# Kernel tuning notes

Measured on AMD Instinct MI355X. Metric: run time of the kernel, lower is better.

The kernel has to match this reference:

```python
import jax, jax.numpy as jnp
import numpy as np

GRID = 256

def _build_edges(g):
    ii, jj = np.meshgrid(np.arange(g), np.arange(g), indexing='ij')
    center = ii * g + jj
    srcs, tgts, attrs = [], [], []
    for di in (-1, 0, 1):
        for dj in (-1, 0, 1):
            if di == 0 and dj == 0:
                continue
            ni, nj = ii + di, jj + dj
            m = (ni >= 0) & (ni < g) & (nj >= 0) & (nj < g)
            srcs.append(center[m])
            tgts.append((ni * g + nj)[m])
            n = int(m.sum())
            a = np.empty((n, 3), np.float32)
            a[:, 0] = np.sqrt(di * di + dj * dj)
            a[:, 1] = di
            a[:, 2] = dj
            attrs.append(a)
    return (np.concatenate(srcs).astype(np.int32),
            np.concatenate(tgts).astype(np.int32),
            np.concatenate(attrs, axis=0))

def setup_inputs() -> dict:
    key = jax.random.key(0)
    ks = jax.random.split(key, 16)
    B, T, C, g = 2, 5, 10, GRID
    width, kw, out_c, Hh = 64, 32, 10, 32
    src, tgt, attr = _build_edges(g)
    nrm = lambda k, s: 0.1 * jax.random.normal(k, s, dtype=jnp.float32)
    return {
        'x': nrm(ks[0], (B, T, C, g, g)),
        'edge_src': jnp.asarray(src),
        'edge_tgt': jnp.asarray(tgt),
        'edge_attr': jnp.asarray(attr),
        'Wih0': nrm(ks[1], (4 * Hh, C)),
        'Whh0': nrm(ks[2], (4 * Hh, Hh)),
        'bih0': nrm(ks[3], (4 * Hh,)),
        'bhh0': nrm(ks[4], (4 * Hh,)),
        'Wih1': nrm(ks[5], (4 * Hh, Hh)),
        'Whh1': nrm(ks[6], (4 * Hh, Hh)),
        'bih1': nrm(ks[7], (4 * Hh,)),
        'bhh1': nrm(ks[8], (4 * Hh,)),
        'fc1_w': nrm(ks[9], (width, Hh)),
        'fc1_b': nrm(ks[10], (width,)),
        'conv_w': nrm(ks[11], (4, width, width)),
        'conv_b': nrm(ks[12], (4, width)),
        'gparam': jnp.ones((4,), jnp.float32),
        'fc2_w': nrm(ks[13], (kw, width)),
        'fc2_b': nrm(ks[14], (kw,)),
        'fc3_w': nrm(ks[15], (out_c, kw)),
        'fc3_b': jnp.zeros((out_c,), jnp.float32),
    }

def _lstm_cell(xt, h, c, Wih, Whh, bih, bhh):
    z = xt @ Wih.T + bih + h @ Whh.T + bhh
    i, f, g, o = jnp.split(z, 4, axis=-1)  # torch gate order i,f,g,o
    c = jax.nn.sigmoid(f) * c + jax.nn.sigmoid(i) * jnp.tanh(g)
    h = jax.nn.sigmoid(o) * jnp.tanh(c)
    return h, c

def _forward(x, edge_src, edge_tgt, edge_attr, Wih0, Whh0, bih0, bhh0,
             Wih1, Whh1, bih1, bhh1, fc1_w, fc1_b, conv_w, conv_b, gparam,
             fc2_w, fc2_b, fc3_w, fc3_b):
    B, T, C, H, W = x.shape
    N = H * W
    Hh = Whh0.shape[1]
    # (B,T,C,H,W) -> (T, B*N, C) sequence for the temporal LSTM over every node
    seq = x.transpose(0, 3, 4, 1, 2).reshape(B * N, T, C).transpose(1, 0, 2)

    def step(carry, xt):
        h0, c0, h1, c1 = carry
        h0, c0 = _lstm_cell(xt, h0, c0, Wih0, Whh0, bih0, bhh0)
        h1, c1 = _lstm_cell(h0, h1, c1, Wih1, Whh1, bih1, bhh1)
        return (h0, c0, h1, c1), None

    z = jnp.zeros((B * N, Hh), x.dtype)
    (h0, c0, h1, c1), _ = jax.lax.scan(step, (z, z, z, z), seq)
    feats = jax.nn.relu(h1 @ fc1_w.T + fc1_b).reshape(B, N, -1)  # (B,N,width)

    dist2 = edge_attr[:, 0:1] ** 2  # (E,1)
    depth = conv_w.shape[0]
    for k in range(depth):
        gw = jnp.exp(-dist2 / (gparam[k] ** 2 + 1e-8))       # (E,1) gaussian gate
        msg = (feats[:, edge_src] @ conv_w[k]) * gw          # (B,E,width)
        agg = jnp.zeros_like(feats).at[:, edge_tgt].add(msg) # scatter-add per batch
        feats = agg + feats @ conv_w[k] + conv_b[k]
        if k != depth - 1:
            feats = jax.nn.relu(feats)

    out = jax.nn.relu(feats @ fc2_w.T + fc2_b) @ fc3_w.T + fc3_b  # (B,N,out_c)
    out = out.reshape(B, H, W, -1).transpose(0, 3, 1, 2)[:, None]  # (B,1,out_c,H,W)
    return out

def reference(x, edge_src, edge_tgt, edge_attr, Wih0, Whh0, bih0, bhh0,
              Wih1, Whh1, bih1, bhh1, fc1_w, fc1_b, conv_w, conv_b, gparam,
              fc2_w, fc2_b, fc3_w, fc3_b):
    return _forward(x, edge_src, edge_tgt, edge_attr, Wih0, Whh0, bih0, bhh0,
                    Wih1, Whh1, bih1, bhh1, fc1_w, fc1_b, conv_w, conv_b, gparam,
                    fc2_w, fc2_b, fc3_w, fc3_b)
```

## Files before the change

### kernel.cpp

```cpp
#include <hip/hip_runtime.h>
#include <hip/hip_bf16.h>

#define NPIX   65536
#define TT     5
#define CC     10
#define HH     32
#define WIDTH  64
#define KW     32
#define OUTC   10

#define OFF_L0I    0
#define OFF_L0H    1280
#define OFF_L1I    5376
#define OFF_L1H    9472
#define OFF_B0     13568
#define OFF_B1     13696
#define OFF_FC1W   13824
#define OFF_FC1B   15872
#define OFF_CWT2   16384
#define OFF_CB     32768
#define OFF_FC2W2  33024
#define OFF_FC2B   35072
#define OFF_FC3W4  35104
#define OFF_FC3B   35424
#define OFF_GW     35440
#define OFF_FEATS_A 36864
#define OFF_FEATS_B (36864 + 8388608)

#define STRAIGHT_ATTR_IDX (65025 * 3)

__device__ __forceinline__ float sigf(float x)  { return 1.0f / (1.0f + __expf(-x)); }
__device__ __forceinline__ float tanhf_(float x){ return 1.0f - 2.0f / (__expf(2.0f * x) + 1.0f); }

__global__ __launch_bounds__(256, 1)
void prep_kernel(const float* Wih0, const float* Whh0,
                 const float* bih0, const float* bhh0,
                 const float* Wih1, const float* Whh1,
                 const float* bih1, const float* bhh1,
                 const float* fc1w, const float* fc1b,
                 const float* convw, const float* convb,
                 const float* fc2w, const float* fc2b,
                 const float* fc3w, const float* fc3b,
                 const float* gparam, const float* eattr,
                 float* P) {
    int tid = blockIdx.x * blockDim.x + threadIdx.x;
    int stride = gridDim.x * blockDim.x;
    for (int idx = tid; idx < 1280; idx += stride) {
        int g = idx & 3, j = (idx >> 2) & 31, c = idx >> 7;
        P[OFF_L0I + idx] = Wih0[(g * 32 + j) * 10 + c];
    }
    for (int idx = tid; idx < 4096; idx += stride) {
        int g = idx & 3, j = (idx >> 2) & 31, k = idx >> 7;
        P[OFF_L0H + idx] = Whh0[(g * 32 + j) * 32 + k];
        P[OFF_L1I + idx] = Wih1[(g * 32 + j) * 32 + k];
        P[OFF_L1H + idx] = Whh1[(g * 32 + j) * 32 + k];
    }
    for (int idx = tid; idx < 128; idx += stride) {
        int g = idx & 3, j = idx >> 2;
        P[OFF_B0 + idx] = bih0[g * 32 + j] + bhh0[g * 32 + j];
        P[OFF_B1 + idx] = bih1[g * 32 + j] + bhh1[g * 32 + j];
    }
    for (int idx = tid; idx < 2048; idx += stride) {
        int ch = idx & 63, k = idx >> 6;
        P[OFF_FC1W + idx] = fc1w[ch * 32 + k];
    }
    for (int i = tid; i < 64; i += stride) P[OFF_FC1B + i] = fc1b[i];
    for (int idx = tid; idx < 16384; idx += stride) {
        int k = idx >> 12, r = idx & 4095, e = r >> 1, h = r & 1;
        int co2 = e >> 6, ci = e & 63;
        P[OFF_CWT2 + idx] = convw[k * 4096 + ci * 64 + (2 * co2 + h)];
    }
    for (int i = tid; i < 256; i += stride) P[OFF_CB + i] = convb[i];
    for (int idx = tid; idx < 2048; idx += stride) {
        int e = idx >> 1, h = idx & 1, m2 = e >> 6, ch = e & 63;
        P[OFF_FC2W2 + idx] = fc2w[(2 * m2 + h) * 64 + ch];
    }
    for (int i = tid; i < 32;  i += stride) P[OFF_FC2B + i] = fc2b[i];
    for (int idx = tid; idx < 320; idx += stride) {
        int q = idx & 3, e = idx >> 2, oc2 = e >> 4, m2 = e & 15;
        int oc = 2 * oc2 + (q & 1), m = 2 * m2 + (q >> 1);
        P[OFF_FC3W4 + idx] = fc3w[oc * 32 + m];
    }
    for (int i = tid; i < 10; i += stride) P[OFF_FC3B + i] = fc3b[i];
    for (int idx = tid; idx < 8; idx += stride) {
        int k = idx >> 1;
        float g = gparam[k];
        float denom = g * g + 1e-8f;
        float a = (idx & 1) ? eattr[0] : eattr[STRAIGHT_ATTR_IDX];
        P[OFF_GW + idx] = __expf(-(a * a) / denom);
    }
}

#define ROW_ACC(WBASE, SVAL) do {                                   \
    const float* wr_ = (WBASE); float sv_ = (SVAL);                 \
    _Pragma("unroll")                                               \
    for (int j_ = 0; j_ < 16; j_++) {                               \
        z[j_].x = __builtin_fmaf(wr_[4 * j_ + 0], sv_, z[j_].x);    \
        z[j_].y = __builtin_fmaf(wr_[4 * j_ + 1], sv_, z[j_].y);    \
        z[j_].z = __builtin_fmaf(wr_[4 * j_ + 2], sv_, z[j_].z);    \
        z[j_].w = __builtin_fmaf(wr_[4 * j_ + 3], sv_, z[j_].w);    \
    } } while (0)

__global__ __launch_bounds__(256, 1)
void lstm_fc1_kernel(const float* __restrict__ x,
                     const float* __restrict__ P,
                     float* __restrict__ feats) {
    __shared__ float H0[HH * 128];
    __shared__ float H1[HH * 128];

    int tid  = threadIdx.x;
    int half = __builtin_amdgcn_readfirstlane(tid >> 7);
    int pxl  = tid & 127;
    int hw   = half << 4;
    int hw4  = half << 6;

    int n = blockIdx.x * 128 + pxl;
    int b = n >> 16;
    int pix = n & (NPIX - 1);
    const float* xb = x + (size_t)b * TT * CC * NPIX + pix;

    float c0[16], c1[16];
#pragma unroll
    for (int j = 0; j < 16; j++) {
        c0[j] = 0.f; c1[j] = 0.f;
        H0[(hw + j) * 128 + pxl] = 0.f;
        H1[(hw + j) * 128 + pxl] = 0.f;
    }
    __syncthreads();

#pragma unroll 1
    for (int t = 0; t < TT; t++) {
        float xcur[CC];
#pragma unroll
        for (int c = 0; c < CC; c++)
            xcur[c] = xb[(size_t)(t * CC + c) * NPIX];

        {
            float4 z[16];
            const float* bb = P + OFF_B0 + hw4;
#pragma unroll
            for (int j = 0; j < 16; j++)
                z[j] = *(const float4*)(bb + 4 * j);
#pragma unroll 1
            for (int c = 0; c < CC; c++)
                ROW_ACC(P + OFF_L0I + c * 128 + hw4, xcur[c]);
#pragma unroll 1
            for (int k = 0; k < HH; k++) {
                float hv = H0[k * 128 + pxl];
                ROW_ACC(P + OFF_L0H + k * 128 + hw4, hv);
            }
            __syncthreads();
#pragma unroll
            for (int j = 0; j < 16; j++) {
                float cn = sigf(z[j].y) * c0[j] + sigf(z[j].x) * tanhf_(z[j].z);
                c0[j] = cn;
                H0[(hw + j) * 128 + pxl] = sigf(z[j].w) * tanhf_(cn);
            }
            __syncthreads();
        }

        {
            float4 z[16];
            const float* bb = P + OFF_B1 + hw4;
#pragma unroll
            for (int j = 0; j < 16; j++)
                z[j] = *(const float4*)(bb + 4 * j);
#pragma unroll 1
            for (int k = 0; k < HH; k++) {
                float hv = H0[k * 128 + pxl];
                ROW_ACC(P + OFF_L1I + k * 128 + hw4, hv);
            }
#pragma unroll 1
            for (int k = 0; k < HH; k++) {
                float hv = H1[k * 128 + pxl];
                ROW_ACC(P + OFF_L1H + k * 128 + hw4, hv);
            }
            __syncthreads();
#pragma unroll
            for (int j = 0; j < 16; j++) {
                float cn = sigf(z[j].y) * c1[j] + sigf(z[j].x) * tanhf_(z[j].z);
                c1[j] = cn;
                H1[(hw + j) * 128 + pxl] = sigf(z[j].w) * tanhf_(cn);
            }
            __syncthreads();
        }
    }

    float f[32];
    {
        const float* fb1 = P + OFF_FC1B + (half << 5);
#pragma unroll
        for (int m = 0; m < 32; m++) f[m] = fb1[m];
    }
#pragma unroll 1
    for (int k = 0; k < HH; k++) {
        float hv = H1[k * 128 + pxl];
        const float* wr = P + OFF_FC1W + k * 64 + (half << 5);
#pragma unroll
        for (int m = 0; m < 32; m++)
            f[m] = __builtin_fmaf(wr[m], hv, f[m]);
    }
    float* fob = feats + (size_t)b * WIDTH * NPIX + (size_t)(half * 32) * NPIX + pix;
#pragma unroll
    for (int m = 0; m < 32; m++)
        fob[(size_t)m * NPIX] = fmaxf(f[m], 0.f);
}

__global__ __launch_bounds__(256, 1)
void conv_fused_kernel(const float* __restrict__ Fin, float* __restrict__ Fout,
                       const float* __restrict__ P, int k) {
    __shared__ float4 CW[1024];
    __shared__ float  CB[64];
    {
        const float4* src = (const float4*)(P + OFF_CWT2 + k * 4096);
        for (int i = threadIdx.x; i < 1024; i += 256) CW[i] = src[i];
        if (threadIdx.x < 64) CB[threadIdx.x] = P[OFF_CB + k * 64 + threadIdx.x];
    }
    __syncthreads();

    int n = blockIdx.x * 256 + threadIdx.x;
    int b = n >> 16;
    int pix = n & (NPIX - 1);
    int i = pix >> 8, j = pix & 255;
    float wstr = P[OFF_GW + 2 * k], wdiag = P[OFF_GW + 2 * k + 1];
    float fu = (i > 0) ? wstr : 0.f, fd = (i < 255) ? wstr : 0.f;
    float fl = (j > 0) ? wstr : 0.f, fr = (j < 255) ? wstr : 0.f;
    float ful = (i > 0 && j > 0) ? wdiag : 0.f, fur = (i > 0 && j < 255) ? wdiag : 0.f;
    float fdl = (i < 255 && j > 0) ? wdiag : 0.f, fdr = (i < 255 && j < 255) ? wdiag : 0.f;

    const float* fb = Fin + (size_t)b * WIDTH * NPIX + pix;
    float u[WIDTH];
#pragma unroll
    for (int ch = 0; ch < WIDTH; ch++) {
        const float* yc = fb + (size_t)ch * NPIX;
        float v = yc[0];
        v += fu * yc[-256] + fd * yc[256] + fl * yc[-1] + fr * yc[1];
        v += ful * yc[-257] + fur * yc[-255] + fdl * yc[255] + fdr * yc[257];
        u[ch] = v;
    }

    float* ob = Fout + (size_t)b * WIDTH * NPIX + pix;
#pragma unroll 1
    for (int co2 = 0; co2 < 32; co2++) {
        float ax = CB[2 * co2], ay = CB[2 * co2 + 1];
        const float4* wv = CW + co2 * 32;
#pragma unroll
        for (int ci2 = 0; ci2 < 32; ci2++) {
            float4 q = wv[ci2];
            float a0 = u[2 * ci2], a1 = u[2 * ci2 + 1];
            ax = __builtin_fmaf(q.x, a0, ax); ax = __builtin_fmaf(q.z, a1, ax);
            ay = __builtin_fmaf(q.y, a0, ay); ay = __builtin_fmaf(q.w, a1, ay);
        }
        ob[(size_t)(2 * co2) * NPIX]     = fmaxf(ax, 0.f);
        ob[(size_t)(2 * co2 + 1) * NPIX] = fmaxf(ay, 0.f);
    }
}

__global__ __launch_bounds__(256, 1)
void conv_head_kernel(const float* __restrict__ Fin, const float* __restrict__ P,
                      float* __restrict__ out) {
    const int k = 3;
    __shared__ float4 CW3[1024];
    __shared__ float  CB3[64];
    __shared__ float4 F2W[512];
    __shared__ float  F2B[32];
    __shared__ float4 F3W[80];
    __shared__ float  F3B[12];
    {
        const float4* s1 = (const float4*)(P + OFF_CWT2 + k * 4096);
        for (int i = threadIdx.x; i < 1024; i += 256) CW3[i] = s1[i];
        const float4* s2 = (const float4*)(P + OFF_FC2W2);
        for (int i = threadIdx.x; i < 512; i += 256) F2W[i] = s2[i];
        const float4* s3 = (const float4*)(P + OFF_FC3W4);
        if (threadIdx.x < 80) F3W[threadIdx.x] = s3[threadIdx.x];
        if (threadIdx.x < 64) CB3[threadIdx.x] = P[OFF_CB + k * 64 + threadIdx.x];
        if (threadIdx.x < 32) F2B[threadIdx.x] = P[OFF_FC2B + threadIdx.x];
        if (threadIdx.x < 10) F3B[threadIdx.x] = P[OFF_FC3B + threadIdx.x];
    }
    __syncthreads();

    int n = blockIdx.x * 256 + threadIdx.x;
    int b = n >> 16;
    int pix = n & (NPIX - 1);
    int i = pix >> 8, j = pix & 255;
    float wstr = P[OFF_GW + 2 * k], wdiag = P[OFF_GW + 2 * k + 1];
    float fu = (i > 0) ? wstr : 0.f, fd = (i < 255) ? wstr : 0.f;
    float fl = (j > 0) ? wstr : 0.f, fr = (j < 255) ? wstr : 0.f;
    float ful = (i > 0 && j > 0) ? wdiag : 0.f, fur = (i > 0 && j < 255) ? wdiag : 0.f;
    float fdl = (i < 255 && j > 0) ? wdiag : 0.f, fdr = (i < 255 && j < 255) ? wdiag : 0.f;

    const float* fb = Fin + (size_t)b * WIDTH * NPIX + pix;
    float u[WIDTH];
#pragma unroll
    for (int ch = 0; ch < WIDTH; ch++) {
        const float* yc = fb + (size_t)ch * NPIX;
        float v = yc[0];
        v += fu * yc[-256] + fd * yc[256] + fl * yc[-1] + fr * yc[1];
        v += ful * yc[-257] + fur * yc[-255] + fdl * yc[255] + fdr * yc[257];
        u[ch] = v;
    }

    float f[WIDTH];
#pragma unroll
    for (int co2 = 0; co2 < 32; co2++) {
        float ax = CB3[2 * co2], ay = CB3[2 * co2 + 1];
        const float4* wv = CW3 + co2 * 32;
#pragma unroll
        for (int ci2 = 0; ci2 < 32; ci2++) {
            float4 q = wv[ci2];
            float a0 = u[2 * ci2], a1 = u[2 * ci2 + 1];
            ax = __builtin_fmaf(q.x, a0, ax); ax = __builtin_fmaf(q.z, a1, ax);
            ay = __builtin_fmaf(q.y, a0, ay); ay = __builtin_fmaf(q.w, a1, ay);
        }
        f[2 * co2] = ax; f[2 * co2 + 1] = ay;
    }

    float2 oo[5];
#pragma unroll
    for (int oc2 = 0; oc2 < 5; oc2++) oo[oc2] = make_float2(F3B[2 * oc2], F3B[2 * oc2 + 1]);
#pragma unroll 1
    for (int m2 = 0; m2 < 16; m2++) {
        float ax = F2B[2 * m2], ay = F2B[2 * m2 + 1];
        const float4* wv = F2W + m2 * 32;
#pragma unroll
        for (int ch2 = 0; ch2 < 32; ch2++) {
            float4 q = wv[ch2];
            ax = __builtin_fmaf(q.x, f[2 * ch2], ax); ax = __builtin_fmaf(q.z, f[2 * ch2 + 1], ax);
            ay = __builtin_fmaf(q.y, f[2 * ch2], ay); ay = __builtin_fmaf(q.w, f[2 * ch2 + 1], ay);
        }
        ax = fmaxf(ax, 0.f); ay = fmaxf(ay, 0.f);
#pragma unroll
        for (int oc2 = 0; oc2 < 5; oc2++) {
            float4 q = F3W[oc2 * 16 + m2];
            oo[oc2].x += q.x * ax + q.z * ay;
            oo[oc2].y += q.y * ax + q.w * ay;
        }
    }
    float* ob = out + (size_t)b * OUTC * NPIX + pix;
#pragma unroll
    for (int oc2 = 0; oc2 < 5; oc2++) {
        ob[(size_t)(2 * oc2) * NPIX]     = oo[oc2].x;
        ob[(size_t)(2 * oc2 + 1) * NPIX] = oo[oc2].y;
    }
}

extern "C" void kernel_launch(void* const* d_in, const int* in_sizes, int n_in,
                              void* d_out, int out_size, void* d_ws, size_t ws_size,
                              hipStream_t stream) {
    const float* x     = (const float*)d_in[0];
    const float* eattr = (const float*)d_in[3];
    const float* Wih0  = (const float*)d_in[4];
    const float* Whh0  = (const float*)d_in[5];
    const float* bih0  = (const float*)d_in[6];
    const float* bhh0  = (const float*)d_in[7];
    const float* Wih1  = (const float*)d_in[8];
    const float* Whh1  = (const float*)d_in[9];
    const float* bih1  = (const float*)d_in[10];
    const float* bhh1  = (const float*)d_in[11];
    const float* fc1w  = (const float*)d_in[12];
    const float* fc1b  = (const float*)d_in[13];
    const float* convw = (const float*)d_in[14];
    const float* convb = (const float*)d_in[15];
    const float* gparam= (const float*)d_in[16];
    const float* fc2w  = (const float*)d_in[17];
    const float* fc2b  = (const float*)d_in[18];
    const float* fc3w  = (const float*)d_in[19];
    const float* fc3b  = (const float*)d_in[20];

    float* P  = (float*)d_ws;
    float* FA = P + OFF_FEATS_A;
    float* FB = P + OFF_FEATS_B;

    prep_kernel<<<64, 256, 0, stream>>>(Wih0, Whh0, bih0, bhh0, Wih1, Whh1, bih1, bhh1,
                                        fc1w, fc1b, convw, convb, fc2w, fc2b, fc3w, fc3b,
                                        gparam, eattr, P);
    lstm_fc1_kernel<<<1024, 256, 0, stream>>>(x, P, FA);
    conv_fused_kernel<<<512, 256, 0, stream>>>(FA, FB, P, 0);
    conv_fused_kernel<<<512, 256, 0, stream>>>(FB, FA, P, 1);
    conv_fused_kernel<<<512, 256, 0, stream>>>(FA, FB, P, 2);
    conv_head_kernel<<<512, 256, 0, stream>>>(FB, P, (float*)d_out);
}
```

Before: 654.5 us.

## Use packed float2 FMAs in LSTM and shrink blocks to 128 threads

The LSTM/fc1 kernel's gate and fc1 accumulations now use 2-wide vector FMA (v2f elementwise fma), which can map to packed FP32 FMA instructions on CDNA. The block size also drops from 256 to 128 threads (64 pixels per block, 2048 blocks), with the shared hidden-state buffers shrunk to match. The aim is to halve the FMA instruction count and allow finer-grained scheduling. The risk is that packed ops need operands in even register pairs, which could add moves, and smaller blocks mean more redundant weight loads.

Result: faster. 600.4 us (-8.3%).

```diff
diff --git a/kernel.cpp b/kernel.cpp
--- a/kernel.cpp
+++ b/kernel.cpp
@@ -29,6 +29,8 @@
 
 #define STRAIGHT_ATTR_IDX (65025 * 3)
 
+typedef float v2f __attribute__((ext_vector_type(2)));
+
 __device__ __forceinline__ float sigf(float x)  { return 1.0f / (1.0f + __expf(-x)); }
 __device__ __forceinline__ float tanhf_(float x){ return 1.0f - 2.0f / (__expf(2.0f * x) + 1.0f); }
 
@@ -91,30 +93,29 @@
     }
 }
 
-#define ROW_ACC(WBASE, SVAL) do {                                   \
-    const float* wr_ = (WBASE); float sv_ = (SVAL);                 \
-    _Pragma("unroll")                                               \
-    for (int j_ = 0; j_ < 16; j_++) {                               \
-        z[j_].x = __builtin_fmaf(wr_[4 * j_ + 0], sv_, z[j_].x);    \
-        z[j_].y = __builtin_fmaf(wr_[4 * j_ + 1], sv_, z[j_].y);    \
-        z[j_].z = __builtin_fmaf(wr_[4 * j_ + 2], sv_, z[j_].z);    \
-        z[j_].w = __builtin_fmaf(wr_[4 * j_ + 3], sv_, z[j_].w);    \
+#define ROW_ACC(WBASE, SVAL) do {                                        \
+    const v2f* wr_ = (const v2f*)(WBASE);                                \
+    float s_ = (SVAL); v2f sv_ = {s_, s_};                               \
+    _Pragma("unroll")                                                    \
+    for (int j_ = 0; j_ < 16; j_++) {                                    \
+        zA[j_] = __builtin_elementwise_fma(wr_[2 * j_],     sv_, zA[j_]);\
+        zB[j_] = __builtin_elementwise_fma(wr_[2 * j_ + 1], sv_, zB[j_]);\
     } } while (0)
 
-__global__ __launch_bounds__(256, 1)
+__global__ __launch_bounds__(128, 1)
 void lstm_fc1_kernel(const float* __restrict__ x,
                      const float* __restrict__ P,
                      float* __restrict__ feats) {
-    __shared__ float H0[HH * 128];
-    __shared__ float H1[HH * 128];
+    __shared__ float H0[HH * 64];
+    __shared__ float H1[HH * 64];
 
     int tid  = threadIdx.x;
-    int half = __builtin_amdgcn_readfirstlane(tid >> 7);
-    int pxl  = tid & 127;
+    int half = __builtin_amdgcn_readfirstlane(tid >> 6);
+    int pxl  = tid & 63;
     int hw   = half << 4;
     int hw4  = half << 6;
 
-    int n = blockIdx.x * 128 + pxl;
+    int n = blockIdx.x * 64 + pxl;
     int b = n >> 16;
     int pix = n & (NPIX - 1);
     const float* xb = x + (size_t)b * TT * CC * NPIX + pix;
@@ -123,8 +124,8 @@
 #pragma unroll
     for (int j = 0; j < 16; j++) {
         c0[j] = 0.f; c1[j] = 0.f;
-        H0[(hw + j) * 128 + pxl] = 0.f;
-        H1[(hw + j) * 128 + pxl] = 0.f;
+        H0[(hw + j) * 64 + pxl] = 0.f;
+        H1[(hw + j) * 64 + pxl] = 0.f;
     }
     __syncthreads();
 
@@ -136,74 +137,81 @@
             xcur[c] = xb[(size_t)(t * CC + c) * NPIX];
 
         {
-            float4 z[16];
-            const float* bb = P + OFF_B0 + hw4;
-#pragma unroll
-            for (int j = 0; j < 16; j++)
-                z[j] = *(const float4*)(bb + 4 * j);
+            v2f zA[16], zB[16];
+            const v2f* bb = (const v2f*)(P + OFF_B0 + hw4);
+#pragma unroll
+            for (int j = 0; j < 16; j++) {
+                zA[j] = bb[2 * j];
+                zB[j] = bb[2 * j + 1];
+            }
 #pragma unroll 1
             for (int c = 0; c < CC; c++)
                 ROW_ACC(P + OFF_L0I + c * 128 + hw4, xcur[c]);
 #pragma unroll 1
             for (int k = 0; k < HH; k++) {
-                float hv = H0[k * 128 + pxl];
+                float hv = H0[k * 64 + pxl];
                 ROW_ACC(P + OFF_L0H + k * 128 + hw4, hv);
             }
             __syncthreads();
 #pragma unroll
             for (int j = 0; j < 16; j++) {
-                float cn = sigf(z[j].y) * c0[j] + sigf(z[j].x) * tanhf_(z[j].z);
+                float cn = sigf(zA[j].y) * c0[j] + sigf(zA[j].x) * tanhf_(zB[j].x);
                 c0[j] = cn;
-                H0[(hw + j) * 128 + pxl] = sigf(z[j].w) * tanhf_(cn);
+                H0[(hw + j) * 64 + pxl] = sigf(zB[j].y) * tanhf_(cn);
             }
             __syncthreads();
         }
 
         {
-            float4 z[16];
-            const float* bb = P + OFF_B1 + hw4;
-#pragma unroll
-            for (int j = 0; j < 16; j++)
-                z[j] = *(const float4*)(bb + 4 * j);
+            v2f zA[16], zB[16];
+            const v2f* bb = (const v2f*)(P + OFF_B1 + hw4);
+#pragma unroll
+            for (int j = 0; j < 16; j++) {
+                zA[j] = bb[2 * j];
+                zB[j] = bb[2 * j + 1];
+            }
 #pragma unroll 1
             for (int k = 0; k < HH; k++) {
-                float hv = H0[k * 128 + pxl];
+                float hv = H0[k * 64 + pxl];
                 ROW_ACC(P + OFF_L1I + k * 128 + hw4, hv);
             }
 #pragma unroll 1
             for (int k = 0; k < HH; k++) {
-                float hv = H1[k * 128 + pxl];
+                float hv = H1[k * 64 + pxl];
                 ROW_ACC(P + OFF_L1H + k * 128 + hw4, hv);
             }
             __syncthreads();
 #pragma unroll
             for (int j = 0; j < 16; j++) {
-                float cn = sigf(z[j].y) * c1[j] + sigf(z[j].x) * tanhf_(z[j].z);
+                float cn = sigf(zA[j].y) * c1[j] + sigf(zA[j].x) * tanhf_(zB[j].x);
                 c1[j] = cn;
-                H1[(hw + j) * 128 + pxl] = sigf(z[j].w) * tanhf_(cn);
+                H1[(hw + j) * 64 + pxl] = sigf(zB[j].y) * tanhf_(cn);
             }
             __syncthreads();
         }
     }
 
-    float f[32];
+    v2f fv[16];
     {
-        const float* fb1 = P + OFF_FC1B + (half << 5);
-#pragma unroll
-        for (int m = 0; m < 32; m++) f[m] = fb1[m];
+        const v2f* fb1 = (const v2f*)(P + OFF_FC1B + (half << 5));
+#pragma unroll
+        for (int m = 0; m < 16; m++) fv[m] = fb1[m];
     }
 #pragma unroll 1
     for (int k = 0; k < HH; k++) {
-        float hv = H1[k * 128 + pxl];
-        const float* wr = P + OFF_FC1W + k * 64 + (half << 5);
-#pragma unroll
-        for (int m = 0; m < 32; m++)
-            f[m] = __builtin_fmaf(wr[m], hv, f[m]);
+        float hv = H1[k * 64 + pxl];
+        v2f h2 = {hv, hv};
+        const v2f* wr = (const v2f*)(P + OFF_FC1W + k * 64 + (half << 5));
+#pragma unroll
+        for (int m = 0; m < 16; m++)
+            fv[m] = __builtin_elementwise_fma(wr[m], h2, fv[m]);
     }
     float* fob = feats + (size_t)b * WIDTH * NPIX + (size_t)(half * 32) * NPIX + pix;
 #pragma unroll
-    for (int m = 0; m < 32; m++)
-        fob[(size_t)m * NPIX] = fmaxf(f[m], 0.f);
+    for (int m = 0; m < 16; m++) {
+        fob[(size_t)(2 * m) * NPIX]     = fmaxf(fv[m].x, 0.f);
+        fob[(size_t)(2 * m + 1) * NPIX] = fmaxf(fv[m].y, 0.f);
+    }
 }
 
 __global__ __launch_bounds__(256, 1)
@@ -374,7 +382,7 @@
     prep_kernel<<<64, 256, 0, stream>>>(Wih0, Whh0, bih0, bhh0, Wih1, Whh1, bih1, bhh1,
                                         fc1w, fc1b, convw, convb, fc2w, fc2b, fc3w, fc3b,
                                         gparam, eattr, P);
-    lstm_fc1_kernel<<<1024, 256, 0, stream>>>(x, P, FA);
+    lstm_fc1_kernel<<<2048, 128, 0, stream>>>(x, P, FA);
     conv_fused_kernel<<<512, 256, 0, stream>>>(FA, FB, P, 0);
     conv_fused_kernel<<<512, 256, 0, stream>>>(FB, FA, P, 1);
     conv_fused_kernel<<<512, 256, 0, stream>>>(FA, FB, P, 2);
```
